# Performance work log

Hardware: AMD Instinct MI355X
Metric: run time of the kernel (lower is better)

## Reference

```python
import jax, jax.numpy as jnp
import numpy as np

D = 1152
H = 16
E = 8
K = 2
MLP_H = int(D * 4.0)
EPS = 1e-6


def _ln(x):
    m = jnp.mean(x, axis=-1, keepdims=True)
    v = jnp.var(x, axis=-1, keepdims=True)
    return (x - m) / jnp.sqrt(v + EPS)


def setup_inputs() -> dict:
    key = jax.random.key(0)
    ks = jax.random.split(key, 16)
    s = lambda k, *sh: (jax.random.normal(k, sh, dtype=jnp.float32) * (1.0 / np.sqrt(sh[-2] if len(sh) > 1 else sh[-1])))
    return {
        "x": jax.random.normal(ks[0], (8, 256, D), dtype=jnp.float32),
        "c": jax.random.normal(ks[1], (8, D), dtype=jnp.float32),
        "qkv_w": s(ks[2], D, 3 * D),
        "qkv_b": jnp.zeros((3 * D,), jnp.float32),
        "proj_w": s(ks[3], D, D),
        "proj_b": jnp.zeros((D,), jnp.float32),
        "adaln_w": s(ks[4], D, 4 * D),
        "adaln_b": jnp.zeros((4 * D,), jnp.float32),
        "gate_w": s(ks[5], D, E),
        "gate_b": jnp.zeros((E,), jnp.float32),
        "w1": s(ks[6], E, D, MLP_H),
        "b1": jnp.zeros((E, MLP_H), jnp.float32),
        "w2": s(ks[7], E, MLP_H, D),
        "b2": jnp.zeros((E, D), jnp.float32),
    }


def _forward(x, c, qkv_w, qkv_b, proj_w, proj_b, adaln_w, adaln_b,
             gate_w, gate_b, w1, b1, w2, b2):
    B, S, _ = x.shape
    hd = D // H
    # adaLN modulation: SiLU -> Linear -> 4 chunks along features
    mod = jax.nn.silu(c) @ adaln_w + adaln_b  # [B, 4D]
    shift_msa, scale_msa, gate_msa, gate_mlp = jnp.split(mod, 4, axis=1)

    # --- attention branch ---
    h = _ln(x) * (1.0 + scale_msa[:, None, :]) + shift_msa[:, None, :]
    qkv = (h @ qkv_w + qkv_b).reshape(B, S, 3, H, hd)
    q, k, v = qkv[:, :, 0], qkv[:, :, 1], qkv[:, :, 2]  # [B,S,H,hd]
    att = jnp.einsum('bqhd,bkhd->bhqk', q, k) * (hd ** -0.5)
    att = jax.nn.softmax(att, axis=-1)
    o = jnp.einsum('bhqk,bkhd->bqhd', att, v).reshape(B, S, D)
    o = o @ proj_w + proj_b
    x = x + gate_msa[:, None, :] * o

    # --- MoE branch ---
    nx = _ln(x).reshape(-1, D)  # [N, D]
    N = nx.shape[0]
    logits = nx @ gate_w + gate_b  # [N, E]
    top_val, top_idx = jax.lax.top_k(logits, K)
    top_score = jax.nn.softmax(top_val, axis=-1)  # softmax over k (dim=1)
    # dense per-token combine weights over experts
    comb = jnp.zeros((N, E), nx.dtype).at[jnp.arange(N)[:, None], top_idx].add(top_score)
    # run every expert on all tokens (same math as masked gather/scatter)
    h1 = jax.nn.gelu(jnp.einsum('nd,edh->enh', nx, w1) + b1[:, None, :], approximate=True)
    eo = jnp.einsum('enh,ehd->end', h1, w2) + b2[:, None, :]  # [E,N,D]
    moe = jnp.einsum('ne,end->nd', comb, eo).reshape(B, S, D)
    return x + gate_mlp[:, None, :] * moe


def reference(x, c, qkv_w, qkv_b, proj_w, proj_b, adaln_w, adaln_b,
              gate_w, gate_b, w1, b1, w2, b2):
    return _forward(x, c, qkv_w, qkv_b, proj_w, proj_b, adaln_w, adaln_b,
                    gate_w, gate_b, w1, b1, w2, b2)
```

## Files before the change

kernel.cpp:

```cpp
#include <hip/hip_runtime.h>
#include <math.h>

#define D_    1152
#define H_    16
#define HD    72
#define E_    8
#define MLPH  4608
#define B_    8
#define S_    256
#define N_TOK 2048

typedef __attribute__((ext_vector_type(8))) short bf16x8;
typedef __attribute__((ext_vector_type(4))) float f32x4;

__device__ __forceinline__ ushort bf_rne(float x) {
    uint u = __float_as_uint(x);
    return (ushort)((u + 0x7FFFu + ((u >> 16) & 1u)) >> 16);
}
__device__ __forceinline__ float bf_f(ushort h) {
    return __uint_as_float(((uint)h) << 16);
}

__global__ __launch_bounds__(256) void wsplit(const float* __restrict__ src,
                                              ushort* __restrict__ hi,
                                              ushort* __restrict__ lo,
                                              int K, int N) {
    size_t off = (size_t)blockIdx.z * K * N;
    src += off; hi += off; lo += off;
    __shared__ float t[32][33];
    int k0 = blockIdx.y * 32, n0 = blockIdx.x * 32;
    int r = threadIdx.x >> 3, cq = (threadIdx.x & 7) * 4;
    float4 v = *(const float4*)&src[(size_t)(k0 + r) * N + n0 + cq];
    t[r][cq + 0] = v.x; t[r][cq + 1] = v.y; t[r][cq + 2] = v.z; t[r][cq + 3] = v.w;
    __syncthreads();
    int n = threadIdx.x >> 3, kq = (threadIdx.x & 7) * 4;
    ushort4 hv, lv;
    {
        float f0 = t[kq + 0][n], f1 = t[kq + 1][n], f2 = t[kq + 2][n], f3 = t[kq + 3][n];
        hv.x = bf_rne(f0); lv.x = bf_rne(f0 - bf_f(hv.x));
        hv.y = bf_rne(f1); lv.y = bf_rne(f1 - bf_f(hv.y));
        hv.z = bf_rne(f2); lv.z = bf_rne(f2 - bf_f(hv.z));
        hv.w = bf_rne(f3); lv.w = bf_rne(f3 - bf_f(hv.w));
    }
    size_t o = (size_t)(n0 + n) * K + k0 + kq;
    *(ushort4*)&hi[o] = hv;
    *(ushort4*)&lo[o] = lv;
}

template<int MODE>
__global__ __launch_bounds__(256) void mfma_gemm(
    const float* __restrict__ A, const ushort* __restrict__ WHg,
    const ushort* __restrict__ WLg, const float* __restrict__ biasg,
    float* __restrict__ C, int M, int N, int K,
    const int* __restrict__ counts, const int* __restrict__ rowmap,
    const int* __restrict__ outmap) {
    int e = (MODE == 0) ? 0 : (int)blockIdx.z;
    int cnt = (MODE == 0) ? M : counts[e];
    int m0 = blockIdx.y * 128;
    if (m0 >= cnt) return;
    int n0 = blockIdx.x * 128;
    const ushort* WH = WHg + (size_t)e * K * N;
    const ushort* WL = WLg + (size_t)e * K * N;
    const float* bias = biasg + (size_t)e * N;

    __shared__ __align__(16) ushort Ah[8][528], Al[8][528], Bh[8][528], Bl[8][528];

    int tid = threadIdx.x;
    int lane = tid & 63, wid = tid >> 6;
    int wr = wid >> 1, wc = wid & 1;

    int ar = tid >> 1, ah = tid & 1;
    const float* arow;
    {
        int p = m0 + ar;
        int g = (MODE == 0) ? p : rowmap[e * N_TOK + (p < cnt ? p : 0)];
        arow = A + (size_t)g * K;
    }
    int afrag = ar >> 4;
    int alm = ar & 15;

    int bnf = tid >> 5, bsub = tid & 31;

    f32x4 acc[4][4];
#pragma unroll
    for (int i = 0; i < 4; ++i)
#pragma unroll
        for (int j = 0; j < 4; ++j) acc[i][j] = (f32x4){0.f, 0.f, 0.f, 0.f};

    for (int k0 = 0; k0 < K; k0 += 32) {
        if (k0) __syncthreads();
        float f[16];
        {
            const float* s = arow + k0 + ah * 16;
            *(float4*)&f[0] = *(const float4*)(s);
            *(float4*)&f[4] = *(const float4*)(s + 4);
            *(float4*)&f[8] = *(const float4*)(s + 8);
            *(float4*)&f[12] = *(const float4*)(s + 12);
        }
#pragma unroll
        for (int grp = 0; grp < 2; ++grp) {
            uint hv[4], lv[4];
#pragma unroll
            for (int jj = 0; jj < 4; ++jj) {
                float v0 = f[grp * 8 + jj * 2], v1 = f[grp * 8 + jj * 2 + 1];
                ushort h0 = bf_rne(v0), h1 = bf_rne(v1);
                ushort l0 = bf_rne(v0 - bf_f(h0)), l1 = bf_rne(v1 - bf_f(h1));
                hv[jj] = (uint)h0 | ((uint)h1 << 16);
                lv[jj] = (uint)l0 | ((uint)l1 << 16);
            }
            int g = ah * 2 + grp;
            int l = g * 16 + alm;
            *(uint4*)&Ah[afrag][l * 8] = make_uint4(hv[0], hv[1], hv[2], hv[3]);
            *(uint4*)&Al[afrag][l * 8] = make_uint4(lv[0], lv[1], lv[2], lv[3]);
        }
#pragma unroll
        for (int s = 0; s < 2; ++s) {
            int l = bsub + s * 32;
            size_t ga = (size_t)(n0 + bnf * 16 + (l & 15)) * K + k0 + 8 * (l >> 4);
            *(uint4*)&Bh[bnf][l * 8] = *(const uint4*)&WH[ga];
            *(uint4*)&Bl[bnf][l * 8] = *(const uint4*)&WL[ga];
        }
        __syncthreads();
        bf16x8 bhv[4], blv[4];
#pragma unroll
        for (int nf = 0; nf < 4; ++nf) {
            int fb = wc * 4 + nf;
            bhv[nf] = *(const bf16x8*)&Bh[fb][lane * 8];
            blv[nf] = *(const bf16x8*)&Bl[fb][lane * 8];
        }
#pragma unroll
        for (int mf = 0; mf < 4; ++mf) {
            int fa = wr * 4 + mf;
            bf16x8 a_h = *(const bf16x8*)&Ah[fa][lane * 8];
            bf16x8 a_l = *(const bf16x8*)&Al[fa][lane * 8];
#pragma unroll
            for (int nf = 0; nf < 4; ++nf) {
                acc[mf][nf] = __builtin_amdgcn_mfma_f32_16x16x32_bf16(a_h, bhv[nf], acc[mf][nf], 0, 0, 0);
                acc[mf][nf] = __builtin_amdgcn_mfma_f32_16x16x32_bf16(a_h, blv[nf], acc[mf][nf], 0, 0, 0);
                acc[mf][nf] = __builtin_amdgcn_mfma_f32_16x16x32_bf16(a_l, bhv[nf], acc[mf][nf], 0, 0, 0);
            }
        }
    }

    int lr = lane >> 4, lc = lane & 15;
    float bv[4];
#pragma unroll
    for (int nf = 0; nf < 4; ++nf) bv[nf] = bias[n0 + wc * 64 + nf * 16 + lc];
#pragma unroll
    for (int mf = 0; mf < 4; ++mf) {
#pragma unroll
        for (int rr = 0; rr < 4; ++rr) {
            int pr = m0 + wr * 64 + mf * 16 + lr * 4 + rr;
            if (MODE != 0 && pr >= cnt) continue;
            size_t orow = (MODE == 0) ? (size_t)pr : (size_t)outmap[e * N_TOK + pr];
            float* crow = C + orow * (size_t)N + n0 + wc * 64 + lc;
#pragma unroll
            for (int nf = 0; nf < 4; ++nf) {
                float v = acc[mf][nf][rr] + bv[nf];
                if (MODE == 1) {
                    float u = 0.7978845608028654f * (v + 0.044715f * v * v * v);
                    v = 0.5f * v * (1.f + tanhf(u));
                }
                crow[nf * 16] = v;
            }
        }
    }
}

__global__ void adaln_kernel(const float* __restrict__ c, const float* __restrict__ w,
                             const float* __restrict__ bias, float* __restrict__ mod) {
    __shared__ float sc[D_];
    int b = blockIdx.y;
    int j = blockIdx.x * 256 + threadIdx.x;
    for (int d = threadIdx.x; d < D_; d += 256) {
        float v = c[b * D_ + d];
        sc[d] = v / (1.f + __expf(-v));
    }
    __syncthreads();
    float acc = bias[j];
    for (int d = 0; d < D_; ++d)
        acc += sc[d] * w[(size_t)d * (4 * D_) + j];
    mod[b * (4 * D_) + j] = acc;
}

__global__ void ln_kernel(const float* __restrict__ x, const float* __restrict__ mod,
                          float* __restrict__ out, int use_mod) {
    int n = blockIdx.x;
    int b = n / S_;
    const float* xr = x + (size_t)n * D_;
    float s = 0.f, s2 = 0.f;
    for (int d = threadIdx.x; d < D_; d += 256) {
        float v = xr[d];
        s += v; s2 += v * v;
    }
    for (int off = 32; off > 0; off >>= 1) {
        s  += __shfl_down(s,  off);
        s2 += __shfl_down(s2, off);
    }
    __shared__ float wsum[4], wsum2[4], stats[2];
    int wid = threadIdx.x >> 6, lane = threadIdx.x & 63;
    if (lane == 0) { wsum[wid] = s; wsum2[wid] = s2; }
    __syncthreads();
    if (threadIdx.x == 0) {
        float ts = 0.f, ts2 = 0.f;
        for (int i = 0; i < 4; ++i) { ts += wsum[i]; ts2 += wsum2[i]; }
        float m = ts / D_;
        float var = ts2 / D_ - m * m;
        stats[0] = m; stats[1] = rsqrtf(var + 1e-6f);
    }
    __syncthreads();
    float m = stats[0], inv = stats[1];
    for (int d = threadIdx.x; d < D_; d += 256) {
        float v = (xr[d] - m) * inv;
        if (use_mod)
            v = v * (1.f + mod[b * (4 * D_) + D_ + d]) + mod[b * (4 * D_) + d];
        out[(size_t)n * D_ + d] = v;
    }
}

__global__ __launch_bounds__(256) void attn_kernel(const float* __restrict__ qkv,
                                                   float* __restrict__ o) {
    int qt = blockIdx.x;
    int hh = blockIdx.y;
    int b  = blockIdx.z;
    __shared__ __align__(16) float Pe[32][257];
    __shared__ __align__(16) float Qs[32][77];
    __shared__ __align__(16) float Ks[32][77];
    __shared__ __align__(16) float Vs[32][76];
    __shared__ __align__(16) float sm[8][32];
    __shared__ __align__(16) float rinv[32];
    int t = threadIdx.x;
    const float scale = 0.11785113019775793f;

    for (int i = t; i < 576; i += 256) {
        int r = i / 18, quad = i % 18;
        int n = b * S_ + qt * 32 + r;
        float4 v = *(const float4*)&qkv[(size_t)n * 3456 + hh * HD + quad * 4];
        Qs[r][quad * 4 + 0] = v.x; Qs[r][quad * 4 + 1] = v.y;
        Qs[r][quad * 4 + 2] = v.z; Qs[r][quad * 4 + 3] = v.w;
    }

    int tx = t & 7, ty = t >> 3;
    for (int c = 0; c < 8; ++c) {
        __syncthreads();
        for (int i = t; i < 576; i += 256) {
            int r = i / 18, quad = i % 18;
            int n = b * S_ + c * 32 + r;
            float4 v = *(const float4*)&qkv[(size_t)n * 3456 + D_ + hh * HD + quad * 4];
            Ks[r][quad * 4 + 0] = v.x; Ks[r][quad * 4 + 1] = v.y;
            Ks[r][quad * 4 + 2] = v.z; Ks[r][quad * 4 + 3] = v.w;
        }
        __syncthreads();
        float a0 = 0.f, a1 = 0.f, a2 = 0.f, a3 = 0.f;
        const float* q_r = &Qs[ty][0];
        const float* k0r = &Ks[tx * 4 + 0][0];
        const float* k1r = &Ks[tx * 4 + 1][0];
        const float* k2r = &Ks[tx * 4 + 2][0];
        const float* k3r = &Ks[tx * 4 + 3][0];
#pragma unroll 8
        for (int dd = 0; dd < HD; ++dd) {
            float qv = q_r[dd];
            a0 += qv * k0r[dd]; a1 += qv * k1r[dd];
            a2 += qv * k2r[dd]; a3 += qv * k3r[dd];
        }
        Pe[ty][c * 32 + tx * 4 + 0] = a0 * scale;
        Pe[ty][c * 32 + tx * 4 + 1] = a1 * scale;
        Pe[ty][c * 32 + tx * 4 + 2] = a2 * scale;
        Pe[ty][c * 32 + tx * 4 + 3] = a3 * scale;
    }
    __syncthreads();

    int r = t & 31, oct = t >> 5;
    float m = -1e30f;
#pragma unroll 8
    for (int k = 0; k < 32; ++k) m = fmaxf(m, Pe[r][oct * 32 + k]);
    sm[oct][r] = m;
    __syncthreads();
    float mm = sm[0][r];
#pragma unroll
    for (int i = 1; i < 8; ++i) mm = fmaxf(mm, sm[i][r]);
    __syncthreads();
    float s = 0.f;
#pragma unroll 8
    for (int k = 0; k < 32; ++k) {
        float e = __expf(Pe[r][oct * 32 + k] - mm);
        Pe[r][oct * 32 + k] = e;
        s += e;
    }
    sm[oct][r] = s;
    __syncthreads();
    if (oct == 0) {
        float ts = 0.f;
#pragma unroll
        for (int i = 0; i < 8; ++i) ts += sm[i][r];
        rinv[r] = 1.f / ts;
    }

    int dq = t & 15, qg = t >> 4;
    int tq = t & 31, tquad = 16 + (t >> 5);
    float4 acc0 = {0.f, 0.f, 0.f, 0.f}, acc1 = {0.f, 0.f, 0.f, 0.f};
    float4 acct = {0.f, 0.f, 0.f, 0.f};
    for (int c = 0; c < 8; ++c) {
        __syncthreads();
        for (int i = t; i < 576; i += 256) {
            int rr = i / 18, quad = i % 18;
            int n = b * S_ + c * 32 + rr;
            float4 v = *(const float4*)&qkv[(size_t)n * 3456 + 2 * D_ + hh * HD + quad * 4];
            *(float4*)&Vs[rr][quad * 4] = v;
        }
        __syncthreads();
#pragma unroll 4
        for (int j = 0; j < 32; ++j) {
            float4 v4 = *(const float4*)&Vs[j][dq * 4];
            float p0 = Pe[qg * 2 + 0][c * 32 + j];
            float p1 = Pe[qg * 2 + 1][c * 32 + j];
            acc0.x += p0 * v4.x; acc0.y += p0 * v4.y;
            acc0.z += p0 * v4.z; acc0.w += p0 * v4.w;
            acc1.x += p1 * v4.x; acc1.y += p1 * v4.y;
            acc1.z += p1 * v4.z; acc1.w += p1 * v4.w;
        }
        if (t < 64) {
#pragma unroll 4
            for (int j = 0; j < 32; ++j) {
                float4 v4 = *(const float4*)&Vs[j][tquad * 4];
                float p = Pe[tq][c * 32 + j];
                acct.x += p * v4.x; acct.y += p * v4.y;
                acct.z += p * v4.z; acct.w += p * v4.w;
            }
        }
    }

    {
        int n0 = b * S_ + qt * 32;
        float ri0 = rinv[qg * 2 + 0], ri1 = rinv[qg * 2 + 1];
        float4 o0, o1;
        o0.x = acc0.x * ri0; o0.y = acc0.y * ri0; o0.z = acc0.z * ri0; o0.w = acc0.w * ri0;
        o1.x = acc1.x * ri1; o1.y = acc1.y * ri1; o1.z = acc1.z * ri1; o1.w = acc1.w * ri1;
        *(float4*)&o[(size_t)(n0 + qg * 2 + 0) * D_ + hh * HD + dq * 4] = o0;
        *(float4*)&o[(size_t)(n0 + qg * 2 + 1) * D_ + hh * HD + dq * 4] = o1;
        if (t < 64) {
            float rit = rinv[tq];
            float4 ot;
            ot.x = acct.x * rit; ot.y = acct.y * rit; ot.z = acct.z * rit; ot.w = acct.w * rit;
            *(float4*)&o[(size_t)(n0 + tq) * D_ + hh * HD + tquad * 4] = ot;
        }
    }
}

__global__ void residual1(const float* __restrict__ x, const float* __restrict__ o2,
                          const float* __restrict__ mod, float* __restrict__ xa) {
    int i = blockIdx.x * 256 + threadIdx.x;
    int n = i / D_, d = i % D_;
    int b = n / S_;
    xa[i] = x[i] + mod[b * (4 * D_) + 2 * D_ + d] * o2[i];
}

__global__ void router_kernel(const float* __restrict__ nx, const float* __restrict__ gw,
                              const float* __restrict__ gb, int* __restrict__ counts,
                              int* __restrict__ etok, int* __restrict__ eslot,
                              int* __restrict__ tslot, float* __restrict__ tscore) {
    int n = blockIdx.x;
    int lane = threadIdx.x;
    float acc[E_] = {};
    for (int d = lane; d < D_; d += 64) {
        float v = nx[(size_t)n * D_ + d];
#pragma unroll
        for (int e = 0; e < E_; ++e) acc[e] += v * gw[d * E_ + e];
    }
#pragma unroll
    for (int e = 0; e < E_; ++e)
        for (int off = 32; off > 0; off >>= 1) acc[e] += __shfl_down(acc[e], off);
    if (lane == 0) {
        float lg[E_];
#pragma unroll
        for (int e = 0; e < E_; ++e) lg[e] = acc[e] + gb[e];
        int i0 = 0;
        for (int e = 1; e < E_; ++e) if (lg[e] > lg[i0]) i0 = e;
        int i1 = -1;
        for (int e = 0; e < E_; ++e) {
            if (e == i0) continue;
            if (i1 < 0 || lg[e] > lg[i1]) i1 = e;
        }
        float e1 = __expf(lg[i1] - lg[i0]);
        float p0 = 1.f / (1.f + e1), p1 = e1 / (1.f + e1);
        int p, slot;
        p = atomicAdd(&counts[i0], 1);
        slot = atomicAdd(&counts[8], 1);
        etok[i0 * N_TOK + p] = n; eslot[i0 * N_TOK + p] = slot;
        tslot[n * 2 + 0] = slot; tscore[n * 2 + 0] = p0;
        p = atomicAdd(&counts[i1], 1);
        slot = atomicAdd(&counts[8], 1);
        etok[i1 * N_TOK + p] = n; eslot[i1 * N_TOK + p] = slot;
        tslot[n * 2 + 1] = slot; tscore[n * 2 + 1] = p1;
    }
}

__global__ void combine_kernel(const float* __restrict__ xa, const float* __restrict__ eo,
                               const float* __restrict__ mod, const int* __restrict__ tslot,
                               const float* __restrict__ tscore, float* __restrict__ out) {
    int i = blockIdx.x * 256 + threadIdx.x;
    int n = i / D_, d = i % D_, b = n / S_;
    int s0 = tslot[n * 2 + 0], s1 = tslot[n * 2 + 1];
    float moe = tscore[n * 2 + 0] * eo[(size_t)s0 * D_ + d] +
                tscore[n * 2 + 1] * eo[(size_t)s1 * D_ + d];
    out[i] = xa[i] + mod[b * (4 * D_) + 3 * D_ + d] * moe;
}

__global__ void zero_counts(int* counts) {
    if (threadIdx.x < 16) counts[threadIdx.x] = 0;
}

extern "C" void kernel_launch(void* const* d_in, const int* in_sizes, int n_in,
                              void* d_out, int out_size, void* d_ws, size_t ws_size,
                              hipStream_t stream) {
    (void)in_sizes; (void)n_in; (void)out_size; (void)ws_size;
    const float* x       = (const float*)d_in[0];
    const float* c       = (const float*)d_in[1];
    const float* qkv_w   = (const float*)d_in[2];
    const float* qkv_b   = (const float*)d_in[3];
    const float* proj_w  = (const float*)d_in[4];
    const float* proj_b  = (const float*)d_in[5];
    const float* adaln_w = (const float*)d_in[6];
    const float* adaln_b = (const float*)d_in[7];
    const float* gate_w  = (const float*)d_in[8];
    const float* gate_b  = (const float*)d_in[9];
    const float* w1      = (const float*)d_in[10];
    const float* b1      = (const float*)d_in[11];
    const float* w2      = (const float*)d_in[12];
    const float* b2      = (const float*)d_in[13];

    float* ws = (float*)d_ws;
    float* mod  = ws;
    float* xa   = ws + 36864;
    float* buf1 = ws + 2396160;
    float* qkvb = ws + 4755456;
    float* atto = ws + 11833344;
    float* o2   = ws + 14192640;
    float* h1   = ws + 4755456;
    float* eo   = ws + 23629824;
    int*   counts = (int*)(ws + 28348416);
    int*   etok   = counts + 16;
    int*   eslot  = etok + 16384;
    int*   tslot  = eslot + 16384;
    float* tscore = (float*)(tslot + 4096);

    ushort* wt = (ushort*)(ws + 28389392);
    ushort* qkvT_hi = wt;
    ushort* qkvT_lo = qkvT_hi + 3981312;
    ushort* projT_hi = qkvT_lo + 3981312;
    ushort* projT_lo = projT_hi + 1327104;
    ushort* w1T_hi = projT_lo + 1327104;
    ushort* w1T_lo = w1T_hi + 42467328;
    ushort* w2T_hi = w1T_lo + 42467328;
    ushort* w2T_lo = w2T_hi + 42467328;

    zero_counts<<<1, 64, 0, stream>>>(counts);
    wsplit<<<dim3(3456 / 32, 1152 / 32, 1), 256, 0, stream>>>(qkv_w, qkvT_hi, qkvT_lo, 1152, 3456);
    wsplit<<<dim3(1152 / 32, 1152 / 32, 1), 256, 0, stream>>>(proj_w, projT_hi, projT_lo, 1152, 1152);
    wsplit<<<dim3(4608 / 32, 1152 / 32, E_), 256, 0, stream>>>(w1, w1T_hi, w1T_lo, 1152, 4608);
    wsplit<<<dim3(1152 / 32, 4608 / 32, E_), 256, 0, stream>>>(w2, w2T_hi, w2T_lo, 4608, 1152);

    adaln_kernel<<<dim3(18, 8), 256, 0, stream>>>(c, adaln_w, adaln_b, mod);
    ln_kernel<<<N_TOK, 256, 0, stream>>>(x, mod, buf1, 1);
    mfma_gemm<0><<<dim3(3456 / 128, N_TOK / 128), 256, 0, stream>>>(
        buf1, qkvT_hi, qkvT_lo, qkv_b, qkvb, N_TOK, 3456, D_, nullptr, nullptr, nullptr);
    attn_kernel<<<dim3(8, H_, B_), 256, 0, stream>>>(qkvb, atto);
    mfma_gemm<0><<<dim3(D_ / 128, N_TOK / 128), 256, 0, stream>>>(
        atto, projT_hi, projT_lo, proj_b, o2, N_TOK, D_, D_, nullptr, nullptr, nullptr);
    residual1<<<(N_TOK * D_) / 256, 256, 0, stream>>>(x, o2, mod, xa);
    ln_kernel<<<N_TOK, 256, 0, stream>>>(xa, nullptr, buf1, 0);
    router_kernel<<<N_TOK, 64, 0, stream>>>(buf1, gate_w, gate_b, counts, etok, eslot,
                                            tslot, tscore);
    mfma_gemm<1><<<dim3(MLPH / 128, N_TOK / 128, E_), 256, 0, stream>>>(
        buf1, w1T_hi, w1T_lo, b1, h1, N_TOK, MLPH, D_, counts, etok, eslot);
    mfma_gemm<2><<<dim3(D_ / 128, N_TOK / 128, E_), 256, 0, stream>>>(
        h1, w2T_hi, w2T_lo, b2, eo, N_TOK, D_, MLPH, counts, eslot, eslot);
    combine_kernel<<<(N_TOK * D_) / 256, 256, 0, stream>>>(xa, eo, mod, tslot, tscore,
                                                           (float*)d_out);
}
```

Measured before the change: 1.498 ms.

## Prefetch GEMM tiles in registers, add split-K and XCD-aware tile remapping

The MFMA GEMM now loads the next K tile of A and B into registers while the current tile's MFMAs run. It writes that tile to LDS after a barrier, so global load latency overlaps compute. The projection and expert down-projection GEMMs are split along K into two partial outputs, which the residual and combine kernels sum, to give more parallel blocks for the short-N shapes. The grid is also flattened and blocks are remapped so each XCD gets a contiguous run of tiles, which should improve L2 reuse. The costs are extra barriers per iteration, higher register pressure, and extra partial-sum traffic written into reused workspace regions.

```diff
diff --git a/kernel.cpp b/kernel.cpp
--- a/kernel.cpp
+++ b/kernel.cpp
@@ -47,21 +47,36 @@
     *(ushort4*)&lo[o] = lv;
 }
 
-template<int MODE>
+template<int MODE, int KS>
 __global__ __launch_bounds__(256) void mfma_gemm(
     const float* __restrict__ A, const ushort* __restrict__ WHg,
     const ushort* __restrict__ WLg, const float* __restrict__ biasg,
-    float* __restrict__ C, int M, int N, int K,
+    float* __restrict__ C, int M, int N, int Ktot,
+    unsigned long long pstride,
     const int* __restrict__ counts, const int* __restrict__ rowmap,
     const int* __restrict__ outmap) {
-    int e = (MODE == 0) ? 0 : (int)blockIdx.z;
+    int zz = (int)blockIdx.z;
+    int kh = (KS == 1) ? 0 : (zz % KS);
+    int e  = (KS == 1) ? zz : (zz / KS);
     int cnt = (MODE == 0) ? M : counts[e];
-    int m0 = blockIdx.y * 128;
+    int NTt = N >> 7;
+    int MTa = (MODE == 0) ? (M >> 7) : ((cnt + 127) >> 7);
+    int nb = NTt * MTa;
+    int bx = (int)blockIdx.x;
+    if (bx >= nb) return;
+    int q = nb >> 3, r = nb & 7;
+    int xcd = bx & 7, ii = bx >> 3;
+    int w = (xcd < r) ? (xcd * (q + 1) + ii) : (r * (q + 1) + (xcd - r) * q + ii);
+    int n0 = (w % NTt) << 7;
+    int m0 = (w / NTt) << 7;
     if (m0 >= cnt) return;
-    int n0 = blockIdx.x * 128;
-    const ushort* WH = WHg + (size_t)e * K * N;
-    const ushort* WL = WLg + (size_t)e * K * N;
+
+    const ushort* WH = WHg + (size_t)e * Ktot * N;
+    const ushort* WL = WLg + (size_t)e * Ktot * N;
     const float* bias = biasg + (size_t)e * N;
+    C += (size_t)kh * pstride;
+    int K = Ktot / KS;
+    int koff = kh * K;
 
     __shared__ __align__(16) ushort Ah[8][528], Al[8][528], Bh[8][528], Bl[8][528];
 
@@ -74,12 +89,16 @@
     {
         int p = m0 + ar;
         int g = (MODE == 0) ? p : rowmap[e * N_TOK + (p < cnt ? p : 0)];
-        arow = A + (size_t)g * K;
+        arow = A + (size_t)g * Ktot;
     }
     int afrag = ar >> 4;
     int alm = ar & 15;
 
     int bnf = tid >> 5, bsub = tid & 31;
+    int brow = n0 + bnf * 16 + (bsub & 15);
+    int bkp  = 8 * (bsub >> 4);
+    const ushort* bhrow = WH + (size_t)brow * Ktot + koff + bkp;
+    const ushort* blrow = WL + (size_t)brow * Ktot + koff + bkp;
 
     f32x4 acc[4][4];
 #pragma unroll
@@ -87,40 +106,50 @@
 #pragma unroll
         for (int j = 0; j < 4; ++j) acc[i][j] = (f32x4){0.f, 0.f, 0.f, 0.f};
 
-    for (int k0 = 0; k0 < K; k0 += 32) {
-        if (k0) __syncthreads();
-        float f[16];
-        {
-            const float* s = arow + k0 + ah * 16;
-            *(float4*)&f[0] = *(const float4*)(s);
-            *(float4*)&f[4] = *(const float4*)(s + 4);
-            *(float4*)&f[8] = *(const float4*)(s + 8);
-            *(float4*)&f[12] = *(const float4*)(s + 12);
-        }
+    float fa[16];
+    uint4 vbh0, vbh1, vbl0, vbl1;
+
+    auto load_tile = [&](int k0) {
+        const float* s = arow + koff + k0 + ah * 16;
+        *(float4*)&fa[0]  = *(const float4*)(s);
+        *(float4*)&fa[4]  = *(const float4*)(s + 4);
+        *(float4*)&fa[8]  = *(const float4*)(s + 8);
+        *(float4*)&fa[12] = *(const float4*)(s + 12);
+        vbh0 = *(const uint4*)(bhrow + k0);
+        vbh1 = *(const uint4*)(bhrow + k0 + 16);
+        vbl0 = *(const uint4*)(blrow + k0);
+        vbl1 = *(const uint4*)(blrow + k0 + 16);
+    };
+    auto stage_write = [&]() {
 #pragma unroll
         for (int grp = 0; grp < 2; ++grp) {
             uint hv[4], lv[4];
 #pragma unroll
             for (int jj = 0; jj < 4; ++jj) {
-                float v0 = f[grp * 8 + jj * 2], v1 = f[grp * 8 + jj * 2 + 1];
+                float v0 = fa[grp * 8 + jj * 2], v1 = fa[grp * 8 + jj * 2 + 1];
                 ushort h0 = bf_rne(v0), h1 = bf_rne(v1);
                 ushort l0 = bf_rne(v0 - bf_f(h0)), l1 = bf_rne(v1 - bf_f(h1));
                 hv[jj] = (uint)h0 | ((uint)h1 << 16);
                 lv[jj] = (uint)l0 | ((uint)l1 << 16);
             }
-            int g = ah * 2 + grp;
-            int l = g * 16 + alm;
+            int l = (ah * 2 + grp) * 16 + alm;
             *(uint4*)&Ah[afrag][l * 8] = make_uint4(hv[0], hv[1], hv[2], hv[3]);
             *(uint4*)&Al[afrag][l * 8] = make_uint4(lv[0], lv[1], lv[2], lv[3]);
         }
-#pragma unroll
-        for (int s = 0; s < 2; ++s) {
-            int l = bsub + s * 32;
-            size_t ga = (size_t)(n0 + bnf * 16 + (l & 15)) * K + k0 + 8 * (l >> 4);
-            *(uint4*)&Bh[bnf][l * 8] = *(const uint4*)&WH[ga];
-            *(uint4*)&Bl[bnf][l * 8] = *(const uint4*)&WL[ga];
-        }
-        __syncthreads();
+        *(uint4*)&Bh[bnf][bsub * 8]        = vbh0;
+        *(uint4*)&Bh[bnf][(bsub + 32) * 8] = vbh1;
+        *(uint4*)&Bl[bnf][bsub * 8]        = vbl0;
+        *(uint4*)&Bl[bnf][(bsub + 32) * 8] = vbl1;
+    };
+
+    int nt = K >> 5;
+    load_tile(0);
+    stage_write();
+    __syncthreads();
+
+    for (int t = 0; t < nt; ++t) {
+        bool more = (t + 1 < nt);
+        if (more) load_tile((t + 1) << 5);
         bf16x8 bhv[4], blv[4];
 #pragma unroll
         for (int nf = 0; nf < 4; ++nf) {
@@ -130,9 +159,9 @@
         }
 #pragma unroll
         for (int mf = 0; mf < 4; ++mf) {
-            int fa = wr * 4 + mf;
-            bf16x8 a_h = *(const bf16x8*)&Ah[fa][lane * 8];
-            bf16x8 a_l = *(const bf16x8*)&Al[fa][lane * 8];
+            int fa2 = wr * 4 + mf;
+            bf16x8 a_h = *(const bf16x8*)&Ah[fa2][lane * 8];
+            bf16x8 a_l = *(const bf16x8*)&Al[fa2][lane * 8];
 #pragma unroll
             for (int nf = 0; nf < 4; ++nf) {
                 acc[mf][nf] = __builtin_amdgcn_mfma_f32_16x16x32_bf16(a_h, bhv[nf], acc[mf][nf], 0, 0, 0);
@@ -140,12 +169,18 @@
                 acc[mf][nf] = __builtin_amdgcn_mfma_f32_16x16x32_bf16(a_l, bhv[nf], acc[mf][nf], 0, 0, 0);
             }
         }
+        if (more) {
+            __syncthreads();
+            stage_write();
+            __syncthreads();
+        }
     }
 
     int lr = lane >> 4, lc = lane & 15;
     float bv[4];
 #pragma unroll
-    for (int nf = 0; nf < 4; ++nf) bv[nf] = bias[n0 + wc * 64 + nf * 16 + lc];
+    for (int nf = 0; nf < 4; ++nf)
+        bv[nf] = (kh == 0) ? bias[n0 + wc * 64 + nf * 16 + lc] : 0.f;
 #pragma unroll
     for (int mf = 0; mf < 4; ++mf) {
 #pragma unroll
@@ -347,12 +382,13 @@
     }
 }
 
-__global__ void residual1(const float* __restrict__ x, const float* __restrict__ o2,
+__global__ void residual1(const float* __restrict__ x, const float* __restrict__ o2a,
+                          const float* __restrict__ o2b,
                           const float* __restrict__ mod, float* __restrict__ xa) {
     int i = blockIdx.x * 256 + threadIdx.x;
     int n = i / D_, d = i % D_;
     int b = n / S_;
-    xa[i] = x[i] + mod[b * (4 * D_) + 2 * D_ + d] * o2[i];
+    xa[i] = x[i] + mod[b * (4 * D_) + 2 * D_ + d] * (o2a[i] + o2b[i]);
 }
 
 __global__ void router_kernel(const float* __restrict__ nx, const float* __restrict__ gw,
@@ -395,14 +431,15 @@
     }
 }
 
-__global__ void combine_kernel(const float* __restrict__ xa, const float* __restrict__ eo,
+__global__ void combine_kernel(const float* __restrict__ xa, const float* __restrict__ eoa,
+                               const float* __restrict__ eob,
                                const float* __restrict__ mod, const int* __restrict__ tslot,
                                const float* __restrict__ tscore, float* __restrict__ out) {
     int i = blockIdx.x * 256 + threadIdx.x;
     int n = i / D_, d = i % D_, b = n / S_;
     int s0 = tslot[n * 2 + 0], s1 = tslot[n * 2 + 1];
-    float moe = tscore[n * 2 + 0] * eo[(size_t)s0 * D_ + d] +
-                tscore[n * 2 + 1] * eo[(size_t)s1 * D_ + d];
+    float moe = tscore[n * 2 + 0] * (eoa[(size_t)s0 * D_ + d] + eob[(size_t)s0 * D_ + d]) +
+                tscore[n * 2 + 1] * (eoa[(size_t)s1 * D_ + d] + eob[(size_t)s1 * D_ + d]);
     out[i] = xa[i] + mod[b * (4 * D_) + 3 * D_ + d] * moe;
 }
 
@@ -453,6 +490,7 @@
     ushort* w1T_lo = w1T_hi + 42467328;
     ushort* w2T_hi = w1T_lo + 42467328;
     ushort* w2T_lo = w2T_hi + 42467328;
+    float* eoB = ws + 28389392;
 
     zero_counts<<<1, 64, 0, stream>>>(counts);
     wsplit<<<dim3(3456 / 32, 1152 / 32, 1), 256, 0, stream>>>(qkv_w, qkvT_hi, qkvT_lo, 1152, 3456);
@@ -462,19 +500,23 @@
 
     adaln_kernel<<<dim3(18, 8), 256, 0, stream>>>(c, adaln_w, adaln_b, mod);
     ln_kernel<<<N_TOK, 256, 0, stream>>>(x, mod, buf1, 1);
-    mfma_gemm<0><<<dim3(3456 / 128, N_TOK / 128), 256, 0, stream>>>(
-        buf1, qkvT_hi, qkvT_lo, qkv_b, qkvb, N_TOK, 3456, D_, nullptr, nullptr, nullptr);
+    mfma_gemm<0, 1><<<dim3(432, 1, 1), 256, 0, stream>>>(
+        buf1, qkvT_hi, qkvT_lo, qkv_b, qkvb, N_TOK, 3456, D_, 0ULL,
+        nullptr, nullptr, nullptr);
     attn_kernel<<<dim3(8, H_, B_), 256, 0, stream>>>(qkvb, atto);
-    mfma_gemm<0><<<dim3(D_ / 128, N_TOK / 128), 256, 0, stream>>>(
-        atto, projT_hi, projT_lo, proj_b, o2, N_TOK, D_, D_, nullptr, nullptr, nullptr);
-    residual1<<<(N_TOK * D_) / 256, 256, 0, stream>>>(x, o2, mod, xa);
+    mfma_gemm<0, 2><<<dim3(144, 1, 2), 256, 0, stream>>>(
+        atto, projT_hi, projT_lo, proj_b, o2, N_TOK, D_, D_, 2359296ULL,
+        nullptr, nullptr, nullptr);
+    residual1<<<(N_TOK * D_) / 256, 256, 0, stream>>>(x, o2, o2 + 2359296, mod, xa);
     ln_kernel<<<N_TOK, 256, 0, stream>>>(xa, nullptr, buf1, 0);
     router_kernel<<<N_TOK, 64, 0, stream>>>(buf1, gate_w, gate_b, counts, etok, eslot,
                                             tslot, tscore);
-    mfma_gemm<1><<<dim3(MLPH / 128, N_TOK / 128, E_), 256, 0, stream>>>(
-        buf1, w1T_hi, w1T_lo, b1, h1, N_TOK, MLPH, D_, counts, etok, eslot);
-    mfma_gemm<2><<<dim3(D_ / 128, N_TOK / 128, E_), 256, 0, stream>>>(
-        h1, w2T_hi, w2T_lo, b2, eo, N_TOK, D_, MLPH, counts, eslot, eslot);
-    combine_kernel<<<(N_TOK * D_) / 256, 256, 0, stream>>>(xa, eo, mod, tslot, tscore,
-                                                           (float*)d_out);
-}
+    mfma_gemm<1, 1><<<dim3(576, 1, E_), 256, 0, stream>>>(
+        buf1, w1T_hi, w1T_lo, b1, h1, N_TOK, MLPH, D_, 0ULL,
+        counts, etok, eslot);
+    mfma_gemm<2, 2><<<dim3(144, 1, E_ * 2), 256, 0, stream>>>(
+        h1, w2T_hi, w2T_lo, b2, eo, N_TOK, D_, MLPH, 4759568ULL,
+        counts, eslot, eslot);
+    combine_kernel<<<(N_TOK * D_) / 256, 256, 0, stream>>>(xa, eo, eoB, mod, tslot,
+                                                           tscore, (float*)d_out);
+}
```

New measurement: 1.372 ms. 1.09x faster.
